# Performance work log

Hardware: AMD Instinct MI355X
Metric: run time of the kernel (lower is better)

Reference implementation:

```python
import jax, jax.numpy as jnp
import numpy as np

N = 100000   # nodes
E = 800000   # edges
IN, H, OUT = 128, 128, 100  # in_channels, hidden_channels, out_channels


def _layernorm(x, g, b, eps=1e-5):
    m = jnp.mean(x, axis=-1, keepdims=True)
    v = jnp.var(x, axis=-1, keepdims=True)
    return (x - m) * jax.lax.rsqrt(v + eps) * g + b


def _sage_mean(x, src, dst, wl, bl, wr, n):
    # PyG SAGEConv(aggr='mean'): lin_l(mean_j x_j) + lin_r(x)
    s = jax.ops.segment_sum(x[src], dst, num_segments=n)               # [n, d]
    cnt = jax.ops.segment_sum(jnp.ones_like(dst, jnp.float32), dst, num_segments=n)
    aggr = s / jnp.maximum(cnt, 1.0)[:, None]
    return aggr @ wl + bl + x @ wr


def _sage_max(x, src, dst, wl, bl, wr, n):
    # PyG SAGEConv(aggr='max'): lin_l(max_j x_j) + lin_r(x); empty segments -> 0
    m = jax.ops.segment_max(x[src], dst, num_segments=n)               # [n, d]
    m = jnp.where(jnp.isfinite(m), m, 0.0)
    return m @ wl + bl + x @ wr


def setup_inputs() -> dict:
    key = jax.random.key(0)
    ks = jax.random.split(key, 16)

    def w(k, shape):
        fan_in = shape[0]
        return jax.random.normal(k, shape, jnp.float32) * (1.0 / np.sqrt(fan_in))

    inp = {
        'x': jax.random.normal(ks[0], (N, IN), jnp.float32),
        'src': jax.random.randint(ks[1], (E,), 0, N, jnp.int32),
        'dst': jax.random.randint(ks[2], (E,), 0, N, jnp.int32),
        's1_wl': w(ks[3], (IN, H)), 's1_bl': jnp.zeros((H,), jnp.float32), 's1_wr': w(ks[4], (IN, H)),
        'ln1_g': jnp.ones((H,), jnp.float32), 'ln1_b': jnp.zeros((H,), jnp.float32),
        's2_wl': w(ks[5], (H, 2 * H)), 's2_bl': jnp.zeros((2 * H,), jnp.float32), 's2_wr': w(ks[6], (H, 2 * H)),
        'ln2_g': jnp.ones((2 * H,), jnp.float32), 'ln2_b': jnp.zeros((2 * H,), jnp.float32),
        's3_wl': w(ks[7], (2 * H, H)), 's3_bl': jnp.zeros((H,), jnp.float32), 's3_wr': w(ks[8], (2 * H, H)),
        'ln3_g': jnp.ones((H,), jnp.float32), 'ln3_b': jnp.zeros((H,), jnp.float32),
        'l1_w': w(ks[9], (H, H // 2)), 'l1_b': jnp.zeros((H // 2,), jnp.float32),
        'ln4_g': jnp.ones((H // 2,), jnp.float32), 'ln4_b': jnp.zeros((H // 2,), jnp.float32),
        'lo_w': w(ks[10], (H // 2, OUT)), 'lo_b': jnp.zeros((OUT,), jnp.float32),
    }
    return inp


def reference(x, src, dst,
              s1_wl, s1_bl, s1_wr, ln1_g, ln1_b,
              s2_wl, s2_bl, s2_wr, ln2_g, ln2_b,
              s3_wl, s3_bl, s3_wr, ln3_g, ln3_b,
              l1_w, l1_b, ln4_g, ln4_b, lo_w, lo_b):
    n = x.shape[0]
    h = _sage_mean(x, src, dst, s1_wl, s1_bl, s1_wr, n)
    h = jax.nn.relu(_layernorm(h, ln1_g, ln1_b))          # dropout disabled (eval)
    h = _sage_max(h, src, dst, s2_wl, s2_bl, s2_wr, n)
    h = jax.nn.relu(_layernorm(h, ln2_g, ln2_b))
    h = _sage_mean(h, src, dst, s3_wl, s3_bl, s3_wr, n)
    h = jax.nn.relu(_layernorm(h, ln3_g, ln3_b))
    h = h @ l1_w + l1_b
    h = jax.nn.relu(_layernorm(h, ln4_g, ln4_b))
    return h @ lo_w + lo_b                                 # [N, OUT]
```

## Files before the change

kernel.cpp:

```cpp
#include <hip/hip_runtime.h>
#include <stdint.h>

#define DEV __device__ __forceinline__

typedef __attribute__((ext_vector_type(8))) short bf16x8;
typedef __attribute__((ext_vector_type(4))) float f32x4;

DEV float bf2f(uint16_t u) { return __uint_as_float(((uint32_t)u) << 16); }
DEV uint16_t f2bfbits(float f) {
    uint32_t x = __float_as_uint(f);
    uint32_t r = x + 0x7fffu + ((x >> 16) & 1u);
    return (uint16_t)(r >> 16);
}
DEV void stv(uint16_t* p, float v) { *p = f2bfbits(v); }
DEV void stv(float* p, float v) { *p = v; }

template<int C> DEV void ldbf(const uint16_t* p, float* f);
template<> DEV void ldbf<2>(const uint16_t* p, float* f) {
    uint32_t v = *reinterpret_cast<const uint32_t*>(p);
    f[0] = __uint_as_float(v << 16); f[1] = __uint_as_float(v & 0xffff0000u);
}
template<> DEV void ldbf<4>(const uint16_t* p, float* f) {
    uint2 v = *reinterpret_cast<const uint2*>(p);
    f[0] = __uint_as_float(v.x << 16); f[1] = __uint_as_float(v.x & 0xffff0000u);
    f[2] = __uint_as_float(v.y << 16); f[3] = __uint_as_float(v.y & 0xffff0000u);
}

DEV void gl16(const uint16_t* g, uint8_t* l) {
    __builtin_amdgcn_global_load_lds(
        (const __attribute__((address_space(1))) uint32_t*)g,
        (__attribute__((address_space(3))) uint32_t*)l, 16, 0, 0);
}

__global__ void k_count(const int* __restrict__ dst, int e, int* __restrict__ deg) {
    int i = blockIdx.x * 256 + threadIdx.x;
    if (i < e) atomicAdd(&deg[dst[i]], 1);
}

__global__ void k_block_sums(const int* __restrict__ deg, int n, int* __restrict__ bsum) {
    __shared__ int sm[256];
    int base = blockIdx.x * 1024;
    int s = 0;
    for (int i = threadIdx.x; i < 1024; i += 256) {
        int g = base + i;
        if (g < n) s += deg[g];
    }
    sm[threadIdx.x] = s; __syncthreads();
    for (int o = 128; o > 0; o >>= 1) {
        if (threadIdx.x < o) sm[threadIdx.x] += sm[threadIdx.x + o];
        __syncthreads();
    }
    if (threadIdx.x == 0) bsum[blockIdx.x] = sm[0];
}

__global__ void k_scan_bsums(int* bsum, int nb) {
    __shared__ int sm[256];
    int t = threadIdx.x;
    int v = (t < nb) ? bsum[t] : 0;
    sm[t] = v; __syncthreads();
    for (int o = 1; o < 256; o <<= 1) {
        int add = (t >= o) ? sm[t - o] : 0;
        __syncthreads();
        sm[t] += add;
        __syncthreads();
    }
    if (t < nb) bsum[t] = (t == 0) ? 0 : sm[t - 1];
}

__global__ void k_scan_final(const int* __restrict__ deg, int n,
                             const int* __restrict__ bsum, int* __restrict__ offs,
                             int* __restrict__ cursor) {
    __shared__ int sm[256];
    int t = threadIdx.x;
    int i0 = blockIdx.x * 1024 + t * 4;
    int d0 = (i0     < n) ? deg[i0]     : 0;
    int d1 = (i0 + 1 < n) ? deg[i0 + 1] : 0;
    int d2 = (i0 + 2 < n) ? deg[i0 + 2] : 0;
    int d3 = (i0 + 3 < n) ? deg[i0 + 3] : 0;
    int ts = d0 + d1 + d2 + d3;
    sm[t] = ts; __syncthreads();
    for (int o = 1; o < 256; o <<= 1) {
        int add = (t >= o) ? sm[t - o] : 0;
        __syncthreads();
        sm[t] += add;
        __syncthreads();
    }
    int e0 = bsum[blockIdx.x] + ((t == 0) ? 0 : sm[t - 1]);
    int e1 = e0 + d0, e2 = e1 + d1, e3 = e2 + d2, e4 = e3 + d3;
    if (i0     < n) { offs[i0]     = e0; cursor[i0]     = e0; }
    if (i0 + 1 < n) { offs[i0 + 1] = e1; cursor[i0 + 1] = e1; }
    if (i0 + 2 < n) { offs[i0 + 2] = e2; cursor[i0 + 2] = e2; }
    if (i0 + 3 < n) { offs[i0 + 3] = e3; cursor[i0 + 3] = e3; }
    if (i0 <= n - 1 && n - 1 < i0 + 4) offs[n] = e4;
}

__global__ void k_scatter(const int* __restrict__ src, const int* __restrict__ dst, int e,
                          int* __restrict__ cursor, int* __restrict__ csr) {
    int i = blockIdx.x * 256 + threadIdx.x;
    if (i < e) {
        int p = atomicAdd(&cursor[dst[i]], 1);
        csr[p] = src[i];
    }
}

__global__ void k_f2b(const float* __restrict__ in, uint16_t* __restrict__ o, int n4) {
    int i = blockIdx.x * 256 + threadIdx.x;
    if (i < n4) {
        float4 v = reinterpret_cast<const float4*>(in)[i];
        uint2 w;
        w.x = f2bfbits(v.x) | ((uint32_t)f2bfbits(v.y) << 16);
        w.y = f2bfbits(v.z) | ((uint32_t)f2bfbits(v.w) << 16);
        reinterpret_cast<uint2*>(o)[i] = w;
    }
}

struct PrepSeg { const float* W; uint16_t* wt; int K, Dreal, koff, ldk, start, end; };
struct PrepAll { PrepSeg s[8]; };

__global__ void k_prep_all(PrepAll P, int total) {
    int idx = blockIdx.x * 256 + threadIdx.x;
    if (idx >= total) return;
#pragma unroll
    for (int i = 0; i < 8; ++i) {
        if (idx >= P.s[i].start && idx < P.s[i].end) {
            int loc = idx - P.s[i].start;
            int K = P.s[i].K;
            int nn = loc / K, k = loc - nn * K;
            float v = (nn < P.s[i].Dreal) ? P.s[i].W[(size_t)k * P.s[i].Dreal + nn] : 0.f;
            P.s[i].wt[(size_t)nn * P.s[i].ldk + P.s[i].koff + k] = f2bfbits(v);
        }
    }
}

template<int D, bool MAXAGG>
__global__ __launch_bounds__(256) void k_aggr(const uint16_t* __restrict__ X,
                                              const int* __restrict__ offs,
                                              const int* __restrict__ csr,
                                              int n, uint16_t* __restrict__ out) {
    constexpr int C = D / 64;
    int lane = threadIdx.x & 63;
    int node = blockIdx.x * 4 + (threadIdx.x >> 6);
    if (node >= n) return;
    int beg = offs[node], end = offs[node + 1];
    float acc[C];
#pragma unroll
    for (int c = 0; c < C; c++) acc[c] = 0.f;
    const size_t loff = (size_t)lane * C;
    int i = beg;
    for (; i + 3 < end; i += 4) {
        int s0 = csr[i], s1 = csr[i + 1], s2 = csr[i + 2], s3 = csr[i + 3];
        float f0[C], f1[C], f2[C], f3[C];
        ldbf<C>(X + (size_t)s0 * D + loff, f0);
        ldbf<C>(X + (size_t)s1 * D + loff, f1);
        ldbf<C>(X + (size_t)s2 * D + loff, f2);
        ldbf<C>(X + (size_t)s3 * D + loff, f3);
#pragma unroll
        for (int c = 0; c < C; c++) {
            if (MAXAGG) {
                acc[c] = fmaxf(acc[c], fmaxf(fmaxf(f0[c], f1[c]), fmaxf(f2[c], f3[c])));
            } else {
                acc[c] += (f0[c] + f1[c]) + (f2[c] + f3[c]);
            }
        }
    }
    for (; i < end; ++i) {
        int s = csr[i];
        float f[C];
        ldbf<C>(X + (size_t)s * D + loff, f);
#pragma unroll
        for (int c = 0; c < C; c++)
            acc[c] = MAXAGG ? fmaxf(acc[c], f[c]) : (acc[c] + f[c]);
    }
    int d = end - beg; if (d < 1) d = 1;
    float scale = MAXAGG ? 1.f : (1.f / (float)d);
    uint16_t* q = out + (size_t)node * D + loff;
    if constexpr (C == 2) {
        uint32_t v = f2bfbits(acc[0] * scale) | ((uint32_t)f2bfbits(acc[1] * scale) << 16);
        *reinterpret_cast<uint32_t*>(q) = v;
    } else {
        uint2 v;
        v.x = f2bfbits(acc[0] * scale) | ((uint32_t)f2bfbits(acc[1] * scale) << 16);
        v.y = f2bfbits(acc[2] * scale) | ((uint32_t)f2bfbits(acc[3] * scale) << 16);
        *reinterpret_cast<uint2*>(q) = v;
    }
}

__global__ __launch_bounds__(256) void k_aggr_ln(const uint16_t* __restrict__ YZ,
                                                 const int* __restrict__ offs,
                                                 const int* __restrict__ csr,
                                                 const float* __restrict__ g,
                                                 const float* __restrict__ b,
                                                 int n, uint16_t* __restrict__ out) {
    int lane = threadIdx.x & 63;
    int node = blockIdx.x * 4 + (threadIdx.x >> 6);
    if (node >= n) return;
    int beg = offs[node], end = offs[node + 1];
    float a0 = 0.f, a1 = 0.f;
    const size_t loff = (size_t)lane * 2;
    int i = beg;
    for (; i + 3 < end; i += 4) {
        int s0 = csr[i], s1 = csr[i + 1], s2 = csr[i + 2], s3 = csr[i + 3];
        float f0[2], f1[2], f2[2], f3[2];
        ldbf<2>(YZ + (size_t)s0 * 256 + loff, f0);
        ldbf<2>(YZ + (size_t)s1 * 256 + loff, f1);
        ldbf<2>(YZ + (size_t)s2 * 256 + loff, f2);
        ldbf<2>(YZ + (size_t)s3 * 256 + loff, f3);
        a0 += (f0[0] + f1[0]) + (f2[0] + f3[0]);
        a1 += (f0[1] + f1[1]) + (f2[1] + f3[1]);
    }
    for (; i < end; ++i) {
        int s = csr[i];
        float f[2];
        ldbf<2>(YZ + (size_t)s * 256 + loff, f);
        a0 += f[0]; a1 += f[1];
    }
    int d = end - beg; if (d < 1) d = 1;
    float scale = 1.f / (float)d;
    float z[2];
    ldbf<2>(YZ + (size_t)node * 256 + 128 + loff, z);
    float v0 = a0 * scale + z[0];
    float v1 = a1 * scale + z[1];
    float s = v0 + v1, s2 = v0 * v0 + v1 * v1;
#pragma unroll
    for (int o = 1; o < 64; o <<= 1) { s += __shfl_xor(s, o); s2 += __shfl_xor(s2, o); }
    float mean = s * (1.f / 128.f);
    float var = s2 * (1.f / 128.f) - mean * mean;
    float inv = rsqrtf(var + 1e-5f);
    float y0 = fmaxf((v0 - mean) * inv * g[loff]     + b[loff],     0.f);
    float y1 = fmaxf((v1 - mean) * inv * g[loff + 1] + b[loff + 1], 0.f);
    uint32_t w = f2bfbits(y0) | ((uint32_t)f2bfbits(y1) << 16);
    *reinterpret_cast<uint32_t*>(out + (size_t)node * 128 + loff) = w;
}

template<int KPER, int DOUT, int DB, bool DUAL, bool LN, bool ZBIAS, typename TO>
__global__ __launch_bounds__(256) void k_mf(const uint16_t* __restrict__ A0,
                                            const uint16_t* __restrict__ A1,
                                            const uint16_t* __restrict__ WT,
                                            const float* __restrict__ bias,
                                            const float* __restrict__ g,
                                            const float* __restrict__ bvec,
                                            int n, TO* __restrict__ out) {
    constexpr int KEFF = KPER * (DUAL ? 2 : 1);
    constexpr int NF = DB / 16;
    constexpr int WPL = DB * 16;
    constexpr int AB = 8192;
    constexpr int WB = DB * 64;
    constexpr int HB = DB / 64;
    __shared__ __align__(16) uint8_t lds[2][AB + WB];

    int tid = threadIdx.x;
    int lane = tid & 63, wid = tid >> 6;
    int lr = lane & 15, kb = lane >> 4;
    int row0 = blockIdx.x * 128;
    int wrow = wid * 32;

    auto stage = [&](int kt, uint8_t* buf) {
        const uint16_t* Asel = A0; int kk = kt;
        if (DUAL && kt >= KPER) { Asel = A1; kk = kt - KPER; }
        uint8_t* aB = buf;
        uint8_t* wB = buf + AB;
#pragma unroll
        for (int j = 0; j < 2; ++j) {
            int p = wid * 2 + j, cb = p >> 1, h = p & 1;
            int grow = row0 + h * 64 + lane; if (grow >= n) grow = n - 1;
            gl16(Asel + (size_t)grow * KPER + kk + cb * 8, aB + cb * 2048 + h * 1024);
        }
#pragma unroll
        for (int j = 0; j < HB; ++j) {
            int p = wid * HB + j, cb = p / HB, h = p % HB;
            int c = h * 64 + lane;
            gl16(WT + (size_t)c * KEFF + kt + cb * 8, wB + cb * WPL + h * 1024);
        }
    };

    f32x4 acc[2][NF] = {};
    stage(0, lds[0]);
    __syncthreads();
    int cur = 0;
    for (int kt = 0; kt < KEFF; kt += 32) {
        if (kt + 32 < KEFF) stage(kt + 32, lds[cur ^ 1]);
        const uint8_t* aB = lds[cur];
        const uint8_t* wB = lds[cur] + AB;
        bf16x8 af0 = *reinterpret_cast<const bf16x8*>(aB + kb * 2048 + (wrow + lr) * 16);
        bf16x8 af1 = *reinterpret_cast<const bf16x8*>(aB + kb * 2048 + (wrow + 16 + lr) * 16);
#pragma unroll
        for (int nf = 0; nf < NF; ++nf) {
            bf16x8 wf = *reinterpret_cast<const bf16x8*>(wB + kb * WPL + (nf * 16 + lr) * 16);
            acc[0][nf] = __builtin_amdgcn_mfma_f32_16x16x32_bf16(af0, wf, acc[0][nf], 0, 0, 0);
            acc[1][nf] = __builtin_amdgcn_mfma_f32_16x16x32_bf16(af1, wf, acc[1][nf], 0, 0, 0);
        }
        __syncthreads();
        cur ^= 1;
    }

#pragma unroll
    for (int nf = 0; nf < NF; ++nf) {
        int col = nf * 16 + lr;
        float bsv;
        if constexpr (ZBIAS) {
            bsv = (col >= DOUT / 2) ? bias[col - DOUT / 2] : 0.f;
        } else {
            bsv = (DB == DOUT || col < DOUT) ? bias[col] : 0.f;
        }
#pragma unroll
        for (int r = 0; r < 4; ++r) { acc[0][nf][r] += bsv; acc[1][nf][r] += bsv; }
    }
    if constexpr (LN) {
        float gv[NF], bv2[NF];
#pragma unroll
        for (int nf = 0; nf < NF; ++nf) {
            int col = nf * 16 + lr;
            gv[nf] = g[col]; bv2[nf] = bvec[col];
        }
#pragma unroll
        for (int m = 0; m < 2; ++m) {
            float s[4], s2[4];
#pragma unroll
            for (int r = 0; r < 4; ++r) { s[r] = 0.f; s2[r] = 0.f; }
#pragma unroll
            for (int nf = 0; nf < NF; ++nf)
#pragma unroll
                for (int r = 0; r < 4; ++r) { float v = acc[m][nf][r]; s[r] += v; s2[r] += v * v; }
#pragma unroll
            for (int r = 0; r < 4; ++r) {
#pragma unroll
                for (int o = 1; o < 16; o <<= 1) {
                    s[r] += __shfl_xor(s[r], o);
                    s2[r] += __shfl_xor(s2[r], o);
                }
                float mean = s[r] / DOUT;
                float var = s2[r] / DOUT - mean * mean;
                float inv = rsqrtf(var + 1e-5f);
#pragma unroll
                for (int nf = 0; nf < NF; ++nf) {
                    float y = (acc[m][nf][r] - mean) * inv * gv[nf] + bv2[nf];
                    acc[m][nf][r] = fmaxf(y, 0.f);
                }
            }
        }
    }
#pragma unroll
    for (int m = 0; m < 2; ++m)
#pragma unroll
        for (int r = 0; r < 4; ++r) {
            int row = row0 + wrow + m * 16 + kb * 4 + r;
            if (row < n) {
#pragma unroll
                for (int nf = 0; nf < NF; ++nf) {
                    int col = nf * 16 + lr;
                    if (DB == DOUT || col < DOUT)
                        stv(out + (size_t)row * DOUT + col, acc[m][nf][r]);
                }
            }
        }
}

extern "C" void kernel_launch(void* const* d_in, const int* in_sizes, int n_in,
                              void* d_out, int out_size, void* d_ws, size_t ws_size,
                              hipStream_t stream) {
    const float* x     = (const float*)d_in[0];
    const int*   src   = (const int*)d_in[1];
    const int*   dst   = (const int*)d_in[2];
    const float* s1_wl = (const float*)d_in[3];
    const float* s1_bl = (const float*)d_in[4];
    const float* s1_wr = (const float*)d_in[5];
    const float* ln1_g = (const float*)d_in[6];
    const float* ln1_b = (const float*)d_in[7];
    const float* s2_wl = (const float*)d_in[8];
    const float* s2_bl = (const float*)d_in[9];
    const float* s2_wr = (const float*)d_in[10];
    const float* ln2_g = (const float*)d_in[11];
    const float* ln2_b = (const float*)d_in[12];
    const float* s3_wl = (const float*)d_in[13];
    const float* s3_bl = (const float*)d_in[14];
    const float* s3_wr = (const float*)d_in[15];
    const float* ln3_g = (const float*)d_in[16];
    const float* ln3_b = (const float*)d_in[17];
    const float* l1_w  = (const float*)d_in[18];
    const float* l1_b  = (const float*)d_in[19];
    const float* ln4_g = (const float*)d_in[20];
    const float* ln4_b = (const float*)d_in[21];
    const float* lo_w  = (const float*)d_in[22];
    const float* lo_b  = (const float*)d_in[23];
    float* out = (float*)d_out;

    const int N = in_sizes[0] / 128;
    const int E = in_sizes[1];
    (void)n_in; (void)out_size; (void)ws_size;

    char* w = (char*)d_ws;
    size_t off = 0;
    auto alloc = [&](size_t bytes) -> void* {
        void* p = w + off;
        off = (off + bytes + 255) & ~(size_t)255;
        return p;
    };
    int* deg    = (int*)alloc((size_t)N * 4);
    int* offs   = (int*)alloc((size_t)(N + 1) * 4);
    int* cursor = (int*)alloc((size_t)N * 4);
    int* bsum   = (int*)alloc(1024 * 4);
    int* csr    = (int*)alloc((size_t)E * 4);
    uint16_t* wt1 = (uint16_t*)alloc(256 * 128 * 2);
    uint16_t* wt2 = (uint16_t*)alloc(256 * 256 * 2);
    uint16_t* wt3 = (uint16_t*)alloc(256 * 256 * 2);
    uint16_t* wt4 = (uint16_t*)alloc(64 * 128 * 2);
    uint16_t* wt5 = (uint16_t*)alloc(128 * 64 * 2);
    uint16_t* xb    = (uint16_t*)alloc((size_t)N * 128 * 2);
    uint16_t* YZ    = (uint16_t*)alloc((size_t)N * 256 * 2);
    uint16_t* h1    = (uint16_t*)alloc((size_t)N * 128 * 2);
    uint16_t* aggrB = (uint16_t*)alloc((size_t)N * 128 * 2);
    uint16_t* h2    = (uint16_t*)alloc((size_t)N * 256 * 2);
    uint16_t* h3    = (uint16_t*)alloc((size_t)N * 128 * 2);
    uint16_t* h4    = aggrB;

    int gE = (E + 255) / 256;
    int nb = (N + 1023) / 1024;
    int gNode = (N + 3) / 4;
    int g128 = (N + 127) / 128;

    hipMemsetAsync(deg, 0, (size_t)N * 4, stream);
    k_count<<<gE, 256, 0, stream>>>(dst, E, deg);
    k_block_sums<<<nb, 256, 0, stream>>>(deg, N, bsum);
    k_scan_bsums<<<1, 256, 0, stream>>>(bsum, nb);
    k_scan_final<<<nb, 256, 0, stream>>>(deg, N, bsum, offs, cursor);
    k_scatter<<<gE, 256, 0, stream>>>(src, dst, E, cursor, csr);

    PrepAll P;
    int cum = 0;
    auto seg = [&](int i, const float* W, uint16_t* wt, int K, int Dreal, int Dpad, int koff, int ldk) {
        P.s[i] = {W, wt, K, Dreal, koff, ldk, cum, cum + Dpad * K};
        cum += Dpad * K;
    };
    seg(0, s1_wl, wt1,             128, 128, 128, 0,   128);
    seg(1, s1_wr, wt1 + 128 * 128, 128, 128, 128, 0,   128);
    seg(2, s2_wl, wt2,             128, 256, 256, 0,   256);
    seg(3, s2_wr, wt2,             128, 256, 256, 128, 256);
    seg(4, s3_wl, wt3,             256, 128, 128, 0,   256);
    seg(5, s3_wr, wt3 + 128 * 256, 256, 128, 128, 0,   256);
    seg(6, l1_w,  wt4,             128, 64,  64,  0,   128);
    seg(7, lo_w,  wt5,             64,  100, 128, 0,   64);
    k_prep_all<<<(cum + 255) / 256, 256, 0, stream>>>(P, cum);

    k_f2b<<<(N * 128 / 4 + 255) / 256, 256, 0, stream>>>(x, xb, N * 128 / 4);

    k_mf<128, 256, 256, false, false, true, uint16_t><<<g128, 256, 0, stream>>>(
        xb, nullptr, wt1, s1_bl, nullptr, nullptr, N, YZ);
    k_aggr_ln<<<gNode, 256, 0, stream>>>(YZ, offs, csr, ln1_g, ln1_b, N, h1);

    k_aggr<128, true><<<gNode, 256, 0, stream>>>(h1, offs, csr, N, aggrB);
    k_mf<128, 256, 256, true, true, false, uint16_t><<<g128, 256, 0, stream>>>(
        aggrB, h1, wt2, s2_bl, ln2_g, ln2_b, N, h2);

    k_mf<256, 256, 256, false, false, true, uint16_t><<<g128, 256, 0, stream>>>(
        h2, nullptr, wt3, s3_bl, nullptr, nullptr, N, YZ);
    k_aggr_ln<<<gNode, 256, 0, stream>>>(YZ, offs, csr, ln3_g, ln3_b, N, h3);

    k_mf<128, 64, 64, false, true, false, uint16_t><<<g128, 256, 0, stream>>>(
        h3, nullptr, wt4, l1_b, ln4_g, ln4_b, N, h4);

    k_mf<64, 100, 128, false, false, false, float><<<g128, 256, 0, stream>>>(
        h4, nullptr, wt5, lo_b, nullptr, nullptr, N, out);
}
```

Baseline: 424.6 us.

## Restructure MFMA GEMM: whole weight in LDS, 8 waves of 64x64 tiles, direct A loads

The GEMM kernel now loads the full transposed weight matrix into LDS once per block and uses 512-thread blocks. Each of the 8 waves computes a 64x64 output tile. A fragments are read straight from global memory into registers, replacing the double-buffered LDS staging and its per-iteration barriers. Row-wise LayerNorm across column-split waves is combined through LDS partial sums. Larger per-block LDS use (up to 128KB for K=256) limits occupancy, and uncoalesced direct A loads may raise memory latency.

```diff
diff --git a/kernel.cpp b/kernel.cpp
--- a/kernel.cpp
+++ b/kernel.cpp
@@ -232,8 +232,8 @@
     *reinterpret_cast<uint32_t*>(out + (size_t)node * 128 + loff) = w;
 }
 
-template<int KPER, int DOUT, int DB, bool DUAL, bool LN, bool ZBIAS, typename TO>
-__global__ __launch_bounds__(256) void k_mf(const uint16_t* __restrict__ A0,
+template<int KPER, int DOUT, int DB, int ROWS, bool DUAL, bool LN, bool ZBIAS, typename TO>
+__global__ __launch_bounds__(512) void k_mf(const uint16_t* __restrict__ A0,
                                             const uint16_t* __restrict__ A1,
                                             const uint16_t* __restrict__ WT,
                                             const float* __restrict__ bias,
@@ -241,61 +241,63 @@
                                             const float* __restrict__ bvec,
                                             int n, TO* __restrict__ out) {
     constexpr int KEFF = KPER * (DUAL ? 2 : 1);
-    constexpr int NF = DB / 16;
+    constexpr int NCW = DB / 64;
+    constexpr int NRW = ROWS / 64;
+    static_assert(NCW * NRW == 8, "8 waves of 64x64");
     constexpr int WPL = DB * 16;
-    constexpr int AB = 8192;
-    constexpr int WB = DB * 64;
-    constexpr int HB = DB / 64;
-    __shared__ __align__(16) uint8_t lds[2][AB + WB];
+    constexpr int NPL = KEFF / 8;
+    constexpr int WHB = DB / 64;
+    constexpr int TCH = NPL * WHB;
+    __shared__ __align__(16) uint8_t wL[NPL * WPL];
 
     int tid = threadIdx.x;
     int lane = tid & 63, wid = tid >> 6;
     int lr = lane & 15, kb = lane >> 4;
-    int row0 = blockIdx.x * 128;
-    int wrow = wid * 32;
-
-    auto stage = [&](int kt, uint8_t* buf) {
-        const uint16_t* Asel = A0; int kk = kt;
-        if (DUAL && kt >= KPER) { Asel = A1; kk = kt - KPER; }
-        uint8_t* aB = buf;
-        uint8_t* wB = buf + AB;
-#pragma unroll
-        for (int j = 0; j < 2; ++j) {
-            int p = wid * 2 + j, cb = p >> 1, h = p & 1;
-            int grow = row0 + h * 64 + lane; if (grow >= n) grow = n - 1;
-            gl16(Asel + (size_t)grow * KPER + kk + cb * 8, aB + cb * 2048 + h * 1024);
-        }
-#pragma unroll
-        for (int j = 0; j < HB; ++j) {
-            int p = wid * HB + j, cb = p / HB, h = p % HB;
-            int c = h * 64 + lane;
-            gl16(WT + (size_t)c * KEFF + kt + cb * 8, wB + cb * WPL + h * 1024);
-        }
-    };
-
-    f32x4 acc[2][NF] = {};
-    stage(0, lds[0]);
+    int row0 = blockIdx.x * ROWS;
+    int wr = wid / NCW, wc = wid % NCW;
+
+    for (int p = wid; p < TCH; p += 8) {
+        int cp = p / WHB, h = p % WHB;
+        gl16(WT + (size_t)(h * 64 + lane) * KEFF + cp * 8, wL + cp * WPL + h * 1024);
+    }
+
+    const uint16_t* arow0[4];
+    const uint16_t* arow1[4];
+#pragma unroll
+    for (int m = 0; m < 4; ++m) {
+        int row = row0 + wr * 64 + m * 16 + lr;
+        if (row >= n) row = n - 1;
+        arow0[m] = A0 + (size_t)row * KPER;
+        if constexpr (DUAL) arow1[m] = A1 + (size_t)row * KPER;
+    }
+
     __syncthreads();
-    int cur = 0;
+
+    f32x4 acc[4][4] = {};
+#pragma unroll
     for (int kt = 0; kt < KEFF; kt += 32) {
-        if (kt + 32 < KEFF) stage(kt + 32, lds[cur ^ 1]);
-        const uint8_t* aB = lds[cur];
-        const uint8_t* wB = lds[cur] + AB;
-        bf16x8 af0 = *reinterpret_cast<const bf16x8*>(aB + kb * 2048 + (wrow + lr) * 16);
-        bf16x8 af1 = *reinterpret_cast<const bf16x8*>(aB + kb * 2048 + (wrow + 16 + lr) * 16);
-#pragma unroll
-        for (int nf = 0; nf < NF; ++nf) {
-            bf16x8 wf = *reinterpret_cast<const bf16x8*>(wB + kb * WPL + (nf * 16 + lr) * 16);
-            acc[0][nf] = __builtin_amdgcn_mfma_f32_16x16x32_bf16(af0, wf, acc[0][nf], 0, 0, 0);
-            acc[1][nf] = __builtin_amdgcn_mfma_f32_16x16x32_bf16(af1, wf, acc[1][nf], 0, 0, 0);
-        }
-        __syncthreads();
-        cur ^= 1;
-    }
-
-#pragma unroll
-    for (int nf = 0; nf < NF; ++nf) {
-        int col = nf * 16 + lr;
+        const int kk = (DUAL && kt >= KPER) ? kt - KPER : kt;
+        bf16x8 af[4], wf[4];
+#pragma unroll
+        for (int m = 0; m < 4; ++m) {
+            const uint16_t* ap = (DUAL && kt >= KPER) ? arow1[m] : arow0[m];
+            af[m] = *reinterpret_cast<const bf16x8*>(ap + kk + kb * 8);
+        }
+#pragma unroll
+        for (int q = 0; q < 4; ++q)
+            wf[q] = *reinterpret_cast<const bf16x8*>(
+                wL + (size_t)((kt >> 3) + kb) * WPL + (wc * 64 + q * 16 + lr) * 16);
+#pragma unroll
+        for (int m = 0; m < 4; ++m)
+#pragma unroll
+            for (int q = 0; q < 4; ++q)
+                acc[m][q] = __builtin_amdgcn_mfma_f32_16x16x32_bf16(af[m], wf[q], acc[m][q], 0, 0, 0);
+    }
+
+    float gv[4], bvv[4];
+#pragma unroll
+    for (int q = 0; q < 4; ++q) {
+        int col = wc * 64 + q * 16 + lr;
         float bsv;
         if constexpr (ZBIAS) {
             bsv = (col >= DOUT / 2) ? bias[col - DOUT / 2] : 0.f;
@@ -303,53 +305,84 @@
             bsv = (DB == DOUT || col < DOUT) ? bias[col] : 0.f;
         }
 #pragma unroll
-        for (int r = 0; r < 4; ++r) { acc[0][nf][r] += bsv; acc[1][nf][r] += bsv; }
+        for (int m = 0; m < 4; ++m)
+#pragma unroll
+            for (int r = 0; r < 4; ++r) acc[m][q][r] += bsv;
+        if constexpr (LN) { gv[q] = g[col]; bvv[q] = bvec[col]; }
     }
     if constexpr (LN) {
-        float gv[NF], bv2[NF];
-#pragma unroll
-        for (int nf = 0; nf < NF; ++nf) {
-            int col = nf * 16 + lr;
-            gv[nf] = g[col]; bv2[nf] = bvec[col];
-        }
-#pragma unroll
-        for (int m = 0; m < 2; ++m) {
-            float s[4], s2[4];
-#pragma unroll
-            for (int r = 0; r < 4; ++r) { s[r] = 0.f; s2[r] = 0.f; }
-#pragma unroll
-            for (int nf = 0; nf < NF; ++nf)
-#pragma unroll
-                for (int r = 0; r < 4; ++r) { float v = acc[m][nf][r]; s[r] += v; s2[r] += v * v; }
-#pragma unroll
-            for (int r = 0; r < 4; ++r) {
+        float sA[4][4], s2A[4][4];
+#pragma unroll
+        for (int m = 0; m < 4; ++m) {
+#pragma unroll
+            for (int r = 0; r < 4; ++r) { sA[m][r] = 0.f; s2A[m][r] = 0.f; }
+#pragma unroll
+            for (int q = 0; q < 4; ++q)
+#pragma unroll
+                for (int r = 0; r < 4; ++r) { float v = acc[m][q][r]; sA[m][r] += v; s2A[m][r] += v * v; }
+#pragma unroll
+            for (int r = 0; r < 4; ++r)
 #pragma unroll
                 for (int o = 1; o < 16; o <<= 1) {
-                    s[r] += __shfl_xor(s[r], o);
-                    s2[r] += __shfl_xor(s2[r], o);
+                    sA[m][r] += __shfl_xor(sA[m][r], o);
+                    s2A[m][r] += __shfl_xor(s2A[m][r], o);
                 }
-                float mean = s[r] / DOUT;
-                float var = s2[r] / DOUT - mean * mean;
-                float inv = rsqrtf(var + 1e-5f);
-#pragma unroll
-                for (int nf = 0; nf < NF; ++nf) {
-                    float y = (acc[m][nf][r] - mean) * inv * gv[nf] + bv2[nf];
-                    acc[m][nf][r] = fmaxf(y, 0.f);
+        }
+        if constexpr (NCW == 1) {
+#pragma unroll
+            for (int m = 0; m < 4; ++m)
+#pragma unroll
+                for (int r = 0; r < 4; ++r) {
+                    float mean = sA[m][r] / DOUT;
+                    float var = s2A[m][r] / DOUT - mean * mean;
+                    float inv = rsqrtf(var + 1e-5f);
+#pragma unroll
+                    for (int q = 0; q < 4; ++q)
+                        acc[m][q][r] = fmaxf((acc[m][q][r] - mean) * inv * gv[q] + bvv[q], 0.f);
                 }
+        } else {
+            float* smS  = reinterpret_cast<float*>(wL);
+            float* smS2 = smS + ROWS * NCW;
+            __syncthreads();
+            if (lr == 0) {
+#pragma unroll
+                for (int m = 0; m < 4; ++m)
+#pragma unroll
+                    for (int r = 0; r < 4; ++r) {
+                        int rg = wr * 64 + m * 16 + kb * 4 + r;
+                        smS[rg * NCW + wc]  = sA[m][r];
+                        smS2[rg * NCW + wc] = s2A[m][r];
+                    }
             }
-        }
-    }
-#pragma unroll
-    for (int m = 0; m < 2; ++m)
+            __syncthreads();
+#pragma unroll
+            for (int m = 0; m < 4; ++m)
+#pragma unroll
+                for (int r = 0; r < 4; ++r) {
+                    int rg = wr * 64 + m * 16 + kb * 4 + r;
+                    float ss = 0.f, ss2 = 0.f;
+#pragma unroll
+                    for (int w2 = 0; w2 < NCW; ++w2) { ss += smS[rg * NCW + w2]; ss2 += smS2[rg * NCW + w2]; }
+                    float mean = ss / DOUT;
+                    float var = ss2 / DOUT - mean * mean;
+                    float inv = rsqrtf(var + 1e-5f);
+#pragma unroll
+                    for (int q = 0; q < 4; ++q)
+                        acc[m][q][r] = fmaxf((acc[m][q][r] - mean) * inv * gv[q] + bvv[q], 0.f);
+                }
+        }
+    }
+#pragma unroll
+    for (int m = 0; m < 4; ++m)
 #pragma unroll
         for (int r = 0; r < 4; ++r) {
-            int row = row0 + wrow + m * 16 + kb * 4 + r;
+            int row = row0 + wr * 64 + m * 16 + kb * 4 + r;
             if (row < n) {
 #pragma unroll
-                for (int nf = 0; nf < NF; ++nf) {
-                    int col = nf * 16 + lr;
+                for (int q = 0; q < 4; ++q) {
+                    int col = wc * 64 + q * 16 + lr;
                     if (DB == DOUT || col < DOUT)
-                        stv(out + (size_t)row * DOUT + col, acc[m][nf][r]);
+                        stv(out + (size_t)row * DOUT + col, acc[m][q][r]);
                 }
             }
         }
@@ -417,6 +450,8 @@
     int nb = (N + 1023) / 1024;
     int gNode = (N + 3) / 4;
     int g128 = (N + 127) / 128;
+    int g256 = (N + 255) / 256;
+    int g512 = (N + 511) / 512;
 
     hipMemsetAsync(deg, 0, (size_t)N * 4, stream);
     k_count<<<gE, 256, 0, stream>>>(dst, E, deg);
@@ -443,21 +478,21 @@
 
     k_f2b<<<(N * 128 / 4 + 255) / 256, 256, 0, stream>>>(x, xb, N * 128 / 4);
 
-    k_mf<128, 256, 256, false, false, true, uint16_t><<<g128, 256, 0, stream>>>(
+    k_mf<128, 256, 256, 128, false, false, true, uint16_t><<<g128, 512, 0, stream>>>(
         xb, nullptr, wt1, s1_bl, nullptr, nullptr, N, YZ);
     k_aggr_ln<<<gNode, 256, 0, stream>>>(YZ, offs, csr, ln1_g, ln1_b, N, h1);
 
     k_aggr<128, true><<<gNode, 256, 0, stream>>>(h1, offs, csr, N, aggrB);
-    k_mf<128, 256, 256, true, true, false, uint16_t><<<g128, 256, 0, stream>>>(
+    k_mf<128, 256, 256, 128, true, true, false, uint16_t><<<g128, 512, 0, stream>>>(
         aggrB, h1, wt2, s2_bl, ln2_g, ln2_b, N, h2);
 
-    k_mf<256, 256, 256, false, false, true, uint16_t><<<g128, 256, 0, stream>>>(
+    k_mf<256, 256, 256, 128, false, false, true, uint16_t><<<g128, 512, 0, stream>>>(
         h2, nullptr, wt3, s3_bl, nullptr, nullptr, N, YZ);
     k_aggr_ln<<<gNode, 256, 0, stream>>>(YZ, offs, csr, ln3_g, ln3_b, N, h3);
 
-    k_mf<128, 64, 64, false, true, false, uint16_t><<<g128, 256, 0, stream>>>(
+    k_mf<128, 64, 64, 512, false, true, false, uint16_t><<<g512, 512, 0, stream>>>(
         h3, nullptr, wt4, l1_b, ln4_g, ln4_b, N, h4);
 
-    k_mf<64, 100, 128, false, false, false, float><<<g128, 256, 0, stream>>>(
+    k_mf<64, 100, 128, 256, false, false, false, float><<<g256, 512, 0, stream>>>(
         h4, nullptr, wt5, lo_b, nullptr, nullptr, N, out);
 }
```

Result: slower. 494.0 us (+16.3%).
